# Kernel optimization log

Hardware: AMD Instinct MI355X
Metric: run time of the kernel (lower is better)

## Reference

```python
import jax, jax.numpy as jnp
import numpy as np

N = 50000        # nodes
E = 800000       # edges (avg degree 16)
F_IN = 128       # num_node_features
HEADS = 4        # const.NUM_HEADS
CH = 32          # const.NUM_CHANNELS
CLS = 40         # num_classes
NEG_SLOPE = 0.2  # PyG GATv2Conv default


def setup_inputs() -> dict:
    key = jax.random.key(0)
    ks = jax.random.split(key, 10)
    x = jax.random.normal(ks[0], (N, F_IN), dtype=jnp.float32)
    edge_index = jax.random.randint(ks[1], (2, E), 0, N, dtype=jnp.int64)
    s1 = 1.0 / np.sqrt(F_IN)
    s2 = 1.0 / np.sqrt(HEADS * CH)
    w1_l = jax.random.normal(ks[2], (F_IN, HEADS * CH), jnp.float32) * s1
    w1_r = jax.random.normal(ks[3], (F_IN, HEADS * CH), jnp.float32) * s1
    a1 = jax.random.normal(ks[4], (HEADS, CH), jnp.float32) * (1.0 / np.sqrt(CH))
    b1 = jnp.zeros((HEADS * CH,), jnp.float32)
    w2_l = jax.random.normal(ks[5], (HEADS * CH, CLS), jnp.float32) * s2
    w2_r = jax.random.normal(ks[6], (HEADS * CH, CLS), jnp.float32) * s2
    a2 = jax.random.normal(ks[7], (1, CLS), jnp.float32) * (1.0 / np.sqrt(CLS))
    b2 = jnp.zeros((CLS,), jnp.float32)
    return {"x": x, "edge_index": edge_index, "w1_l": w1_l, "w1_r": w1_r,
            "a1": a1, "b1": b1, "w2_l": w2_l, "w2_r": w2_r, "a2": a2, "b2": b2}


def _gatv2_conv(x, src, dst, wl, wr, a, b, concat):
    """GATv2Conv (PyG semantics, eval mode: no dropout).
    src -> lin_l, dst -> lin_r; e = a . LeakyReLU(x_l[src] + x_r[dst]);
    segment softmax over dst; out_i = sum_j alpha * x_l[src]."""
    H, C = a.shape
    n = x.shape[0]
    xl = (x @ wl).reshape(n, H, C)
    xr = (x @ wr).reshape(n, H, C)
    # per-edge additive attention logits [E, H]
    e = jnp.einsum('ehc,hc->eh', jax.nn.leaky_relu(xl[src] + xr[dst], NEG_SLOPE), a)
    # numerically stable segment softmax over target nodes
    m = jax.ops.segment_max(e, dst, num_segments=n)          # [n, H]
    p = jnp.exp(e - m[dst])
    denom = jax.ops.segment_sum(p, dst, num_segments=n)     # [n, H]
    alpha = p / denom[dst]
    out = jax.ops.segment_sum(alpha[..., None] * xl[src], dst, num_segments=n)  # [n, H, C]
    out = out.reshape(n, H * C) if concat else out.mean(axis=1)
    return out + b


def reference(x, edge_index, w1_l, w1_r, a1, b1, w2_l, w2_r, a2, b2):
    n = x.shape[0]
    # PyG GATv2Conv default add_self_loops=True
    loop = jnp.arange(n, dtype=edge_index.dtype)
    src = jnp.concatenate([edge_index[0], loop])
    dst = jnp.concatenate([edge_index[1], loop])
    h = jax.nn.elu(_gatv2_conv(x, src, dst, w1_l, w1_r, a1, b1, concat=True))
    # F.dropout with training=False is identity
    out = _gatv2_conv(h, src, dst, w2_l, w2_r, a2, b2, concat=False)
    return jax.nn.log_softmax(out, axis=1)
```

## Files before the change

### kernel.cpp

```cpp
#include <hip/hip_runtime.h>
#include <hip/hip_bf16.h>
#include <math.h>

#define NN 50000
#define NE 800000
#define ETOT (NE + NN)
#define CLS 40
#define CLSP 48
#define NEG 0.2f
#define MTILES (NN / 16)
#define GB1 ((MTILES + 3) / 4)
#define PREPB 176
#define NBUCK 196
#define BCAP 8192
#define EB 4096
#define KAB ((ETOT + EB - 1) / EB)

#define L2E 1.44269504088896f
#define C06 (0.6f * L2E)
#define C04 (0.4f * L2E)

typedef __hip_bfloat16 bf16;
typedef __attribute__((ext_vector_type(8))) __bf16 bf16x8;
typedef __attribute__((ext_vector_type(4))) float f32x4;
typedef __attribute__((ext_vector_type(2))) float f32x2;
struct U3 { unsigned x, y, z; };

__device__ __forceinline__ bf16x8 cvt8(f32x4 a, f32x4 b) {
    bf16x8 r;
    r[0] = (__bf16)a[0]; r[1] = (__bf16)a[1]; r[2] = (__bf16)a[2]; r[3] = (__bf16)a[3];
    r[4] = (__bf16)b[0]; r[5] = (__bf16)b[1]; r[6] = (__bf16)b[2]; r[7] = (__bf16)b[3];
    return r;
}
__device__ __forceinline__ f32x2 unpk2(unsigned u) {
    f32x2 r;
    r.x = __uint_as_float(u << 16);
    r.y = __uint_as_float(u & 0xffff0000u);
    return r;
}

__device__ __forceinline__ unsigned scan256(unsigned v, unsigned* wsum) {
    int t = threadIdx.x;
    int lane = t & 63, w = t >> 6;
    unsigned inc = v;
#pragma unroll
    for (int d = 1; d < 64; d <<= 1) {
        unsigned x = __shfl_up(inc, d);
        if (lane >= d) inc += x;
    }
    if (lane == 63) wsum[w] = inc;
    __syncthreads();
    unsigned woff = 0;
#pragma unroll
    for (int i = 0; i < 4; i++) woff += (i < w) ? wsum[i] : 0;
    return woff + inc - v;
}

__global__ __launch_bounds__(256) void prep(
        const float* __restrict__ w1l, const float* __restrict__ w1r,
        const float* __restrict__ w2l, const float* __restrict__ w2r,
        bf16* __restrict__ wT1, bf16* __restrict__ wT2,
        int* __restrict__ bcursor) {
    int t = blockIdx.x * 256 + threadIdx.x;
    if (t < NBUCK) bcursor[t] = 0;
    if (t < 2 * 128 * 128) {
        int m = t >> 14;
        int idx = t & 16383;
        int n = idx >> 7, k = idx & 127;
        const float* w = m ? w1r : w1l;
        wT1[t] = __float2bfloat16(w[k * 128 + n]);
    } else if (t < 2 * 128 * 128 + 2 * CLSP * 128) {
        int u = t - 2 * 128 * 128;
        int m = u / (CLSP * 128);
        int idx = u % (CLSP * 128);
        int n = idx >> 7, k = idx & 127;
        const float* w = m ? w2r : w2l;
        wT2[u] = __float2bfloat16((n < CLS) ? w[k * CLS + n] : 0.0f);
    }
}

__global__ __launch_bounds__(256) void gemm1_scatter(
        const float* __restrict__ x, const bf16* __restrict__ wT,
        bf16* __restrict__ outL, bf16* __restrict__ outR,
        const int* __restrict__ ei, int* __restrict__ bcursor,
        uint2* __restrict__ tmp) {
    __shared__ unsigned hist[256];
    __shared__ unsigned lstart[256];
    __shared__ unsigned lcur[256];
    __shared__ unsigned gbase[256];
    __shared__ unsigned wsum[4];
    __shared__ uint2 binned[EB];
    __shared__ unsigned target[EB];
    if ((int)blockIdx.x < GB1) {
        int wave = threadIdx.x >> 6;
        int lane = threadIdx.x & 63;
        int tile = blockIdx.x * 4 + wave;
        if (tile >= MTILES) return;
        const bf16* wl = wT;
        const bf16* wr = wT + 128 * 128;
        int row0 = tile * 16;
        int l16 = lane & 15, quad = lane >> 4;
        f32x4 z = {0.f, 0.f, 0.f, 0.f};
        f32x4 accl[8], accr[8];
#pragma unroll
        for (int i = 0; i < 8; i++) { accl[i] = z; accr[i] = z; }
        const float* xrow = x + (size_t)(row0 + l16) * 128 + quad * 8;
#pragma unroll
        for (int k0 = 0; k0 < 128; k0 += 32) {
            f32x4 a0 = *reinterpret_cast<const f32x4*>(xrow + k0);
            f32x4 a1v = *reinterpret_cast<const f32x4*>(xrow + k0 + 4);
            bf16x8 a = cvt8(a0, a1v);
#pragma unroll
            for (int ct = 0; ct < 8; ct++) {
                bf16x8 bl = *reinterpret_cast<const bf16x8*>(wl + (ct * 16 + l16) * 128 + k0 + quad * 8);
                bf16x8 br = *reinterpret_cast<const bf16x8*>(wr + (ct * 16 + l16) * 128 + k0 + quad * 8);
                accl[ct] = __builtin_amdgcn_mfma_f32_16x16x32_bf16(a, bl, accl[ct], 0, 0, 0);
                accr[ct] = __builtin_amdgcn_mfma_f32_16x16x32_bf16(a, br, accr[ct], 0, 0, 0);
            }
        }
#pragma unroll
        for (int ct = 0; ct < 8; ct++)
#pragma unroll
            for (int r = 0; r < 4; r++) {
                size_t o = (size_t)(row0 + quad * 4 + r) * 128 + ct * 16 + l16;
                outL[o] = __float2bfloat16(accl[ct][r]);
                outR[o] = __float2bfloat16(accr[ct][r]);
            }
    } else {
        int t = threadIdx.x;
        int e0 = (blockIdx.x - GB1) * EB;
        hist[t] = 0;
        __syncthreads();
        int srcs[16], dsts[16];
#pragma unroll
        for (int i = 0; i < 16; i++) {
            int e = e0 + i * 256 + t;
            if (e < ETOT) {
                int s, d;
                if (e < NE) { s = ei[e]; d = ei[NE + e]; }
                else        { s = d = e - NE; }
                srcs[i] = s; dsts[i] = d;
                atomicAdd(&hist[d >> 8], 1u);
            } else dsts[i] = -1;
        }
        __syncthreads();
        unsigned v = hist[t];
        unsigned excl = scan256(v, wsum);
        lstart[t] = excl;
        lcur[t] = 0;
        __syncthreads();
        if (t < NBUCK && v > 0)
            gbase[t] = (unsigned)atomicAdd(&bcursor[t], (int)v) + (unsigned)t * BCAP;
        __syncthreads();
#pragma unroll
        for (int i = 0; i < 16; i++) {
            int d = dsts[i];
            if (d >= 0) {
                int bk = d >> 8;
                unsigned p = atomicAdd(&lcur[bk], 1u);
                unsigned slot = lstart[bk] + p;
                binned[slot] = make_uint2((unsigned)srcs[i], (unsigned)d);
                target[slot] = gbase[bk] + p;
            }
        }
        __syncthreads();
        int tot = min(EB, ETOT - e0);
        for (int s = t; s < tot; s += 256)
            tmp[target[s]] = binned[s];
    }
}

__global__ __launch_bounds__(256) void bucket_sort(const int* __restrict__ bcursor,
                                                   const uint2* __restrict__ tmp,
                                                   int* __restrict__ csr_src,
                                                   int* __restrict__ startA,
                                                   int* __restrict__ degA) {
    __shared__ unsigned hist[256];
    __shared__ unsigned lcur[256];
    __shared__ unsigned wsum[4];
    int b = blockIdx.x, t = threadIdx.x;
    int cnt = bcursor[b];
    hist[t] = 0;
    __syncthreads();
    const uint2* seg = tmp + (size_t)b * BCAP;
    for (int s = t; s < cnt; s += 256)
        atomicAdd(&hist[seg[s].y & 255], 1u);
    __syncthreads();
    unsigned v = hist[t];
    unsigned excl = scan256(v, wsum);
    lcur[t] = excl;
    int node = b * 256 + t;
    if (node < NN) {
        startA[node] = b * BCAP + (int)excl;
        degA[node] = (int)v;
    }
    __syncthreads();
    int* cbase = csr_src + (size_t)b * BCAP;
    for (int s = t; s < cnt; s += 256) {
        uint2 p = seg[s];
        unsigned pos = atomicAdd(&lcur[p.y & 255], 1u);
        cbase[pos] = (int)p.x;
    }
}

struct L1S { float s; f32x2 acc[4]; };
__device__ __forceinline__ void l1_consume(uint4 u, bool valid, const f32x2* xrp,
                                           const f32x2* a06, const float* a04, L1S& st) {
    f32x2 t0 = unpk2(u.x) + xrp[0];
    f32x2 t1 = unpk2(u.y) + xrp[1];
    f32x2 t2 = unpk2(u.z) + xrp[2];
    f32x2 t3 = unpk2(u.w) + xrp[3];
    f32x2 ep = t0 * a06[0];
    ep = __builtin_elementwise_fma(t1, a06[1], ep);
    ep = __builtin_elementwise_fma(t2, a06[2], ep);
    ep = __builtin_elementwise_fma(t3, a06[3], ep);
    float e0 = fmaf(a04[1], fabsf(t0.y), a04[0] * fabsf(t0.x));
    e0 = fmaf(a04[2], fabsf(t1.x), e0);
    e0 = fmaf(a04[3], fabsf(t1.y), e0);
    float e1 = fmaf(a04[5], fabsf(t2.y), a04[4] * fabsf(t2.x));
    e1 = fmaf(a04[6], fabsf(t3.x), e1);
    e1 = fmaf(a04[7], fabsf(t3.y), e1);
    float e = (ep.x + ep.y) + (e0 + e1);
    e += __shfl_xor(e, 1);
    e += __shfl_xor(e, 2);
    float w = valid ? __builtin_amdgcn_exp2f(e) : 0.f;
    st.s += w;
    f32x2 wv = {w, w};
    st.acc[0] = __builtin_elementwise_fma(wv, t0, st.acc[0]);
    st.acc[1] = __builtin_elementwise_fma(wv, t1, st.acc[1]);
    st.acc[2] = __builtin_elementwise_fma(wv, t2, st.acc[2]);
    st.acc[3] = __builtin_elementwise_fma(wv, t3, st.acc[3]);
}

__global__ __launch_bounds__(256) void node_l1(const int* __restrict__ startA,
                                               const int* __restrict__ degA,
                                               const int* __restrict__ csr_src,
                                               const bf16* __restrict__ xl,
                                               const bf16* __restrict__ xr,
                                               const float* __restrict__ a1,
                                               const float* __restrict__ b1,
                                               bf16* __restrict__ hb) {
    int wid = (blockIdx.x * 256 + threadIdx.x) >> 6;
    int lane = threadIdx.x & 63;
    int g = lane >> 4, t = lane & 15;
    unsigned cB = (unsigned)t * 16;
    int j0 = startA[wid];
    int deg = degA[wid];
    unsigned rowB = (unsigned)csr_src[j0 + min(lane, deg - 1)] << 8;
    const char* xlb = (const char*)xl;
    f32x2 xrp[4];
    {
        uint4 raw = *(const uint4*)((const char*)xr + ((unsigned)wid << 8) + cB);
        xrp[0] = unpk2(raw.x); xrp[1] = unpk2(raw.y);
        xrp[2] = unpk2(raw.z); xrp[3] = unpk2(raw.w);
    }
    f32x2 a06[4];
    float a04[8];
    {
        f32x4 lo = *reinterpret_cast<const f32x4*>(a1 + t * 8);
        f32x4 hi = *reinterpret_cast<const f32x4*>(a1 + t * 8 + 4);
        float af[8];
#pragma unroll
        for (int k = 0; k < 4; k++) { af[k] = lo[k]; af[k + 4] = hi[k]; }
#pragma unroll
        for (int j = 0; j < 4; j++) {
            a06[j].x = af[2 * j] * C06;
            a06[j].y = af[2 * j + 1] * C06;
        }
#pragma unroll
        for (int k = 0; k < 8; k++) a04[k] = af[k] * C04;
    }
    L1S st; st.s = 0.f;
    f32x2 z2 = {0.f, 0.f};
#pragma unroll
    for (int k = 0; k < 4; k++) st.acc[k] = z2;
    int nb = (deg + 3) >> 2;
    uint4 u[8];
#pragma unroll
    for (int i = 0; i < 4; i++) {
        int pp = min(i * 4 + g, deg - 1);
        u[i] = *(const uint4*)(xlb + (__shfl(rowB, pp) + cB));
    }
    if (nb > 4) {
#pragma unroll
        for (int i = 4; i < 8; i++) {
            int pp = min(i * 4 + g, deg - 1);
            u[i] = *(const uint4*)(xlb + (__shfl(rowB, pp) + cB));
        }
    }
    l1_consume(u[0], g < deg, xrp, a06, a04, st);
    if (nb > 1) l1_consume(u[1], 4 + g < deg, xrp, a06, a04, st);
    if (nb > 2) l1_consume(u[2], 8 + g < deg, xrp, a06, a04, st);
    if (nb > 3) l1_consume(u[3], 12 + g < deg, xrp, a06, a04, st);
    if (nb > 4) {
        l1_consume(u[4], 16 + g < deg, xrp, a06, a04, st);
        if (nb > 5) l1_consume(u[5], 20 + g < deg, xrp, a06, a04, st);
        if (nb > 6) l1_consume(u[6], 24 + g < deg, xrp, a06, a04, st);
        if (nb > 7) l1_consume(u[7], 28 + g < deg, xrp, a06, a04, st);
        for (int b = 8; b < nb; b++) {
            int p = b * 4 + g;
            bool valid = p < deg;
            int pp = valid ? p : deg - 1;
            unsigned o = __shfl(rowB, min(pp, 63)) + cB;
            if (pp >= 64) o = (((unsigned)csr_src[j0 + pp]) << 8) + cB;
            uint4 uu = *(const uint4*)(xlb + o);
            l1_consume(uu, valid, xrp, a06, a04, st);
        }
    }
#pragma unroll
    for (int d = 16; d < 64; d <<= 1) {
        st.s += __shfl_xor(st.s, d);
#pragma unroll
        for (int k = 0; k < 4; k++) {
            st.acc[k].x += __shfl_xor(st.acc[k].x, d);
            st.acc[k].y += __shfl_xor(st.acc[k].y, d);
        }
    }
    if (g == 0) {
        float inv = 1.f / st.s;
        unsigned pk[4];
#pragma unroll
        for (int k = 0; k < 4; k++) {
            float o0 = st.acc[k].x * inv - xrp[k].x + b1[t * 8 + 2 * k];
            float o1 = st.acc[k].y * inv - xrp[k].y + b1[t * 8 + 2 * k + 1];
            o0 = o0 > 0.f ? o0 : __expf(o0) - 1.f;
            o1 = o1 > 0.f ? o1 : __expf(o1) - 1.f;
            bf16 r0 = __float2bfloat16(o0), r1 = __float2bfloat16(o1);
            pk[k] = (unsigned)*reinterpret_cast<unsigned short*>(&r0) |
                    ((unsigned)*reinterpret_cast<unsigned short*>(&r1) << 16);
        }
        uint4 w4 = {pk[0], pk[1], pk[2], pk[3]};
        *(uint4*)((char*)hb + ((unsigned)wid << 8) + cB) = w4;
    }
}

__global__ __launch_bounds__(256) void gemm2(const bf16* __restrict__ h,
                                             const bf16* __restrict__ wT,
                                             bf16* __restrict__ outL,
                                             bf16* __restrict__ outR) {
    int wave = threadIdx.x >> 6;
    int lane = threadIdx.x & 63;
    int tile = blockIdx.x * 4 + wave;
    if (tile >= MTILES) return;
    const bf16* wl = wT;
    const bf16* wr = wT + CLSP * 128;
    int row0 = tile * 16;
    int l16 = lane & 15, quad = lane >> 4;
    f32x4 z = {0.f, 0.f, 0.f, 0.f};
    f32x4 accl[3], accr[3];
#pragma unroll
    for (int i = 0; i < 3; i++) { accl[i] = z; accr[i] = z; }
    const bf16* hrow = h + (size_t)(row0 + l16) * 128 + quad * 8;
#pragma unroll
    for (int k0 = 0; k0 < 128; k0 += 32) {
        bf16x8 a = *reinterpret_cast<const bf16x8*>(hrow + k0);
#pragma unroll
        for (int ct = 0; ct < 3; ct++) {
            bf16x8 bl = *reinterpret_cast<const bf16x8*>(wl + (ct * 16 + l16) * 128 + k0 + quad * 8);
            bf16x8 br = *reinterpret_cast<const bf16x8*>(wr + (ct * 16 + l16) * 128 + k0 + quad * 8);
            accl[ct] = __builtin_amdgcn_mfma_f32_16x16x32_bf16(a, bl, accl[ct], 0, 0, 0);
            accr[ct] = __builtin_amdgcn_mfma_f32_16x16x32_bf16(a, br, accr[ct], 0, 0, 0);
        }
    }
#pragma unroll
    for (int ct = 0; ct < 3; ct++)
#pragma unroll
        for (int r = 0; r < 4; r++) {
            size_t o = (size_t)(row0 + quad * 4 + r) * CLSP + ct * 16 + l16;
            outL[o] = __float2bfloat16(accl[ct][r]);
            outR[o] = __float2bfloat16(accr[ct][r]);
        }
}

struct L2S { float s; f32x2 acc[3]; };
__device__ __forceinline__ void l2_consume(U3 u, bool valid, const f32x2* xrp,
                                           const f32x2* a06, const float* a04, L2S& st) {
    f32x2 t0 = unpk2(u.x) + xrp[0];
    f32x2 t1 = unpk2(u.y) + xrp[1];
    f32x2 t2 = unpk2(u.z) + xrp[2];
    f32x2 ep = t0 * a06[0];
    ep = __builtin_elementwise_fma(t1, a06[1], ep);
    ep = __builtin_elementwise_fma(t2, a06[2], ep);
    float es = fmaf(a04[1], fabsf(t0.y), a04[0] * fabsf(t0.x));
    es = fmaf(a04[2], fabsf(t1.x), es);
    es = fmaf(a04[3], fabsf(t1.y), es);
    es = fmaf(a04[4], fabsf(t2.x), es);
    es = fmaf(a04[5], fabsf(t2.y), es);
    float e = (ep.x + ep.y) + es;
    e += __shfl_xor(e, 1);
    e += __shfl_xor(e, 2);
    e += __shfl_xor(e, 4);
    float w = valid ? __builtin_amdgcn_exp2f(e) : 0.f;
    st.s += w;
    f32x2 wv = {w, w};
    st.acc[0] = __builtin_elementwise_fma(wv, t0, st.acc[0]);
    st.acc[1] = __builtin_elementwise_fma(wv, t1, st.acc[1]);
    st.acc[2] = __builtin_elementwise_fma(wv, t2, st.acc[2]);
}

__global__ __launch_bounds__(256) void node_l2(const int* __restrict__ startA,
                                               const int* __restrict__ degA,
                                               const int* __restrict__ csr_src,
                                               const bf16* __restrict__ xl2,
                                               const bf16* __restrict__ xr2,
                                               const float* __restrict__ a2,
                                               const float* __restrict__ b2,
                                               float* __restrict__ out) {
    int wid = (blockIdx.x * 256 + threadIdx.x) >> 6;
    int lane = threadIdx.x & 63;
    int g = lane >> 3, t = lane & 7;
    unsigned cB = (unsigned)t * 12;
    int j0 = startA[wid];
    int deg = degA[wid];
    unsigned rowB = (unsigned)csr_src[j0 + min(lane, deg - 1)] * 96u;
    const char* xlb = (const char*)xl2;
    f32x2 xrp[3];
    {
        U3 raw = *(const U3*)((const char*)xr2 + (unsigned)wid * 96u + cB);
        xrp[0] = unpk2(raw.x); xrp[1] = unpk2(raw.y); xrp[2] = unpk2(raw.z);
    }
    int c = t * 6;
    f32x2 a06[3];
    float a04[6];
#pragma unroll
    for (int k = 0; k < 6; k++) {
        float av = (c + k < CLS) ? a2[c + k] : 0.f;
        a04[k] = av * C04;
        if (k & 1) a06[k >> 1].y = av * C06; else a06[k >> 1].x = av * C06;
    }
    L2S st; st.s = 0.f;
    f32x2 z2 = {0.f, 0.f};
#pragma unroll
    for (int k = 0; k < 3; k++) st.acc[k] = z2;
    int nb = (deg + 7) >> 3;
    U3 u[4];
#pragma unroll
    for (int i = 0; i < 2; i++) {
        int pp = min(i * 8 + g, deg - 1);
        u[i] = *(const U3*)(xlb + (__shfl(rowB, pp) + cB));
    }
    if (nb > 2) {
#pragma unroll
        for (int i = 2; i < 4; i++) {
            int pp = min(i * 8 + g, deg - 1);
            u[i] = *(const U3*)(xlb + (__shfl(rowB, pp) + cB));
        }
    }
    l2_consume(u[0], g < deg, xrp, a06, a04, st);
    if (nb > 1) l2_consume(u[1], 8 + g < deg, xrp, a06, a04, st);
    if (nb > 2) {
        l2_consume(u[2], 16 + g < deg, xrp, a06, a04, st);
        if (nb > 3) l2_consume(u[3], 24 + g < deg, xrp, a06, a04, st);
        for (int b = 4; b < nb; b++) {
            int p = b * 8 + g;
            bool valid = p < deg;
            int pp = valid ? p : deg - 1;
            unsigned o = __shfl(rowB, min(pp, 63)) + cB;
            if (pp >= 64) o = (unsigned)csr_src[j0 + pp] * 96u + cB;
            U3 uu = *(const U3*)(xlb + o);
            l2_consume(uu, valid, xrp, a06, a04, st);
        }
    }
#pragma unroll
    for (int d = 8; d < 64; d <<= 1) {
        st.s += __shfl_xor(st.s, d);
#pragma unroll
        for (int k = 0; k < 3; k++) {
            st.acc[k].x += __shfl_xor(st.acc[k].x, d);
            st.acc[k].y += __shfl_xor(st.acc[k].y, d);
        }
    }
    float inv = 1.f / st.s;
    float q[6];
    float mx = -3e38f;
#pragma unroll
    for (int k = 0; k < 6; k++) {
        bool val = (c + k < CLS);
        float av = (k & 1) ? st.acc[k >> 1].y : st.acc[k >> 1].x;
        float xv = (k & 1) ? xrp[k >> 1].y : xrp[k >> 1].x;
        q[k] = val ? (av * inv - xv + b2[c + k]) : -3e38f;
        mx = fmaxf(mx, q[k]);
    }
    mx = fmaxf(mx, __shfl_xor(mx, 1));
    mx = fmaxf(mx, __shfl_xor(mx, 2));
    mx = fmaxf(mx, __shfl_xor(mx, 4));
    float se = 0.f;
#pragma unroll
    for (int k = 0; k < 6; k++) if (c + k < CLS) se += __expf(q[k] - mx);
    se += __shfl_xor(se, 1);
    se += __shfl_xor(se, 2);
    se += __shfl_xor(se, 4);
    float ls = mx + __logf(se);
    if (g == 0) {
        float* o = out + (size_t)wid * CLS + c;
#pragma unroll
        for (int k = 0; k < 6; k++)
            if (c + k < CLS) o[k] = q[k] - ls;
    }
}

extern "C" void kernel_launch(void* const* d_in, const int* in_sizes, int n_in,
                              void* d_out, int out_size, void* d_ws, size_t ws_size,
                              hipStream_t stream) {
    const float* x   = (const float*)d_in[0];
    const int*   ei  = (const int*)d_in[1];
    const float* w1l = (const float*)d_in[2];
    const float* w1r = (const float*)d_in[3];
    const float* a1  = (const float*)d_in[4];
    const float* b1  = (const float*)d_in[5];
    const float* w2l = (const float*)d_in[6];
    const float* w2r = (const float*)d_in[7];
    const float* a2  = (const float*)d_in[8];
    const float* b2  = (const float*)d_in[9];
    float* out = (float*)d_out;

    char* base = (char*)d_ws;
    int*   bcursor = (int*)(base + 0);
    int*   startA  = (int*)(base + 1024);
    int*   degA    = (int*)(base + 201024);
    uint2* tmp     = (uint2*)(base + 401024);
    int*   csr_src = (int*)(base + 13246080);
    bf16*  xl1     = (bf16*)(base + 19668608);
    bf16*  hb      = (bf16*)(base + 45268608);
    bf16*  xl2p    = (bf16*)(base + 58068608);
    bf16*  wT1     = (bf16*)(base + 67668608);
    bf16*  wT2     = (bf16*)(base + 67734144);
    bf16* xr1  = xl1 + (size_t)NN * 128;
    bf16* xr2p = xl2p + (size_t)NN * CLSP;

    prep<<<PREPB, 256, 0, stream>>>(w1l, w1r, w2l, w2r, wT1, wT2, bcursor);
    gemm1_scatter<<<GB1 + KAB, 256, 0, stream>>>(x, wT1, xl1, xr1, ei, bcursor, tmp);
    bucket_sort<<<NBUCK, 256, 0, stream>>>(bcursor, tmp, csr_src, startA, degA);
    node_l1<<<(NN * 64) / 256, 256, 0, stream>>>(startA, degA, csr_src, xl1, xr1, a1, b1, hb);
    gemm2<<<GB1, 256, 0, stream>>>(hb, wT2, xl2p, xr2p);
    node_l2<<<(NN * 64) / 256, 256, 0, stream>>>(startA, degA, csr_src, xl2p, xr2p, a2, b2, out);
}
```

Before: 231.3 us.

## Make node aggregation kernels persistent with software-pipelined prefetch of next node

Both per-node attention/aggregation kernels now launch a fixed grid of 8192 waves that loop over nodes with stride NW. The next node's CSR metadata, source indices, xr row and first neighbor gathers are prefetched while the current node is consumed and reduced, hiding gather latency. Bias values are hoisted into registers once per wave. This cuts launch/setup overhead and overlaps memory latency, at the cost of higher register pressure and possible load imbalance across waves.

```diff
diff --git a/kernel.cpp b/kernel.cpp
--- a/kernel.cpp
+++ b/kernel.cpp
@@ -15,6 +15,7 @@
 #define BCAP 8192
 #define EB 4096
 #define KAB ((ETOT + EB - 1) / EB)
+#define NW 8192
 
 #define L2E 1.44269504088896f
 #define C06 (0.6f * L2E)
@@ -240,28 +241,24 @@
                                                const float* __restrict__ a1,
                                                const float* __restrict__ b1,
                                                bf16* __restrict__ hb) {
-    int wid = (blockIdx.x * 256 + threadIdx.x) >> 6;
+    int wv = (blockIdx.x * 256 + threadIdx.x) >> 6;
     int lane = threadIdx.x & 63;
     int g = lane >> 4, t = lane & 15;
     unsigned cB = (unsigned)t * 16;
-    int j0 = startA[wid];
-    int deg = degA[wid];
-    unsigned rowB = (unsigned)csr_src[j0 + min(lane, deg - 1)] << 8;
     const char* xlb = (const char*)xl;
-    f32x2 xrp[4];
-    {
-        uint4 raw = *(const uint4*)((const char*)xr + ((unsigned)wid << 8) + cB);
-        xrp[0] = unpk2(raw.x); xrp[1] = unpk2(raw.y);
-        xrp[2] = unpk2(raw.z); xrp[3] = unpk2(raw.w);
-    }
     f32x2 a06[4];
-    float a04[8];
+    float a04[8], bv[8];
     {
         f32x4 lo = *reinterpret_cast<const f32x4*>(a1 + t * 8);
         f32x4 hi = *reinterpret_cast<const f32x4*>(a1 + t * 8 + 4);
+        f32x4 blo = *reinterpret_cast<const f32x4*>(b1 + t * 8);
+        f32x4 bhi = *reinterpret_cast<const f32x4*>(b1 + t * 8 + 4);
         float af[8];
 #pragma unroll
-        for (int k = 0; k < 4; k++) { af[k] = lo[k]; af[k + 4] = hi[k]; }
+        for (int k = 0; k < 4; k++) {
+            af[k] = lo[k]; af[k + 4] = hi[k];
+            bv[k] = blo[k]; bv[k + 4] = bhi[k];
+        }
 #pragma unroll
         for (int j = 0; j < 4; j++) {
             a06[j].x = af[2 * j] * C06;
@@ -270,67 +267,90 @@
 #pragma unroll
         for (int k = 0; k < 8; k++) a04[k] = af[k] * C04;
     }
-    L1S st; st.s = 0.f;
-    f32x2 z2 = {0.f, 0.f};
-#pragma unroll
-    for (int k = 0; k < 4; k++) st.acc[k] = z2;
-    int nb = (deg + 3) >> 2;
+    int n = wv;
+    int j0 = startA[n], deg = degA[n];
+    unsigned rowB = (unsigned)csr_src[j0 + min(lane, deg - 1)] << 8;
+    uint4 xrw = *(const uint4*)((const char*)xr + ((unsigned)n << 8) + cB);
     uint4 u[8];
 #pragma unroll
-    for (int i = 0; i < 4; i++) {
-        int pp = min(i * 4 + g, deg - 1);
-        u[i] = *(const uint4*)(xlb + (__shfl(rowB, pp) + cB));
-    }
-    if (nb > 4) {
-#pragma unroll
-        for (int i = 4; i < 8; i++) {
-            int pp = min(i * 4 + g, deg - 1);
-            u[i] = *(const uint4*)(xlb + (__shfl(rowB, pp) + cB));
-        }
-    }
-    l1_consume(u[0], g < deg, xrp, a06, a04, st);
-    if (nb > 1) l1_consume(u[1], 4 + g < deg, xrp, a06, a04, st);
-    if (nb > 2) l1_consume(u[2], 8 + g < deg, xrp, a06, a04, st);
-    if (nb > 3) l1_consume(u[3], 12 + g < deg, xrp, a06, a04, st);
-    if (nb > 4) {
-        l1_consume(u[4], 16 + g < deg, xrp, a06, a04, st);
-        if (nb > 5) l1_consume(u[5], 20 + g < deg, xrp, a06, a04, st);
-        if (nb > 6) l1_consume(u[6], 24 + g < deg, xrp, a06, a04, st);
-        if (nb > 7) l1_consume(u[7], 28 + g < deg, xrp, a06, a04, st);
-        for (int b = 8; b < nb; b++) {
-            int p = b * 4 + g;
-            bool valid = p < deg;
-            int pp = valid ? p : deg - 1;
-            unsigned o = __shfl(rowB, min(pp, 63)) + cB;
-            if (pp >= 64) o = (((unsigned)csr_src[j0 + pp]) << 8) + cB;
-            uint4 uu = *(const uint4*)(xlb + o);
-            l1_consume(uu, valid, xrp, a06, a04, st);
-        }
-    }
-#pragma unroll
-    for (int d = 16; d < 64; d <<= 1) {
-        st.s += __shfl_xor(st.s, d);
-#pragma unroll
-        for (int k = 0; k < 4; k++) {
-            st.acc[k].x += __shfl_xor(st.acc[k].x, d);
-            st.acc[k].y += __shfl_xor(st.acc[k].y, d);
-        }
-    }
-    if (g == 0) {
-        float inv = 1.f / st.s;
-        unsigned pk[4];
-#pragma unroll
-        for (int k = 0; k < 4; k++) {
-            float o0 = st.acc[k].x * inv - xrp[k].x + b1[t * 8 + 2 * k];
-            float o1 = st.acc[k].y * inv - xrp[k].y + b1[t * 8 + 2 * k + 1];
-            o0 = o0 > 0.f ? o0 : __expf(o0) - 1.f;
-            o1 = o1 > 0.f ? o1 : __expf(o1) - 1.f;
-            bf16 r0 = __float2bfloat16(o0), r1 = __float2bfloat16(o1);
-            pk[k] = (unsigned)*reinterpret_cast<unsigned short*>(&r0) |
-                    ((unsigned)*reinterpret_cast<unsigned short*>(&r1) << 16);
-        }
-        uint4 w4 = {pk[0], pk[1], pk[2], pk[3]};
-        *(uint4*)((char*)hb + ((unsigned)wid << 8) + cB) = w4;
+    for (int i = 0; i < 4; i++)
+        u[i] = *(const uint4*)(xlb + (__shfl(rowB, min(i * 4 + g, deg - 1)) + cB));
+
+    for (;;) {
+        int n2 = n + NW;
+        bool has2 = n2 < NN;
+        int j0b = 0, degb = 1;
+        unsigned rowBb = 0;
+        uint4 xrwb = {0, 0, 0, 0};
+        if (has2) {
+            j0b = startA[n2]; degb = degA[n2];
+            rowBb = (unsigned)csr_src[j0b + min(lane, degb - 1)] << 8;
+            xrwb = *(const uint4*)((const char*)xr + ((unsigned)n2 << 8) + cB);
+        }
+        int nb = (deg + 3) >> 2;
+        if (nb > 4) {
+#pragma unroll
+            for (int i = 4; i < 8; i++)
+                u[i] = *(const uint4*)(xlb + (__shfl(rowB, min(i * 4 + g, deg - 1)) + cB));
+        }
+        f32x2 xrp[4];
+        xrp[0] = unpk2(xrw.x); xrp[1] = unpk2(xrw.y);
+        xrp[2] = unpk2(xrw.z); xrp[3] = unpk2(xrw.w);
+        L1S st; st.s = 0.f;
+        f32x2 z2 = {0.f, 0.f};
+#pragma unroll
+        for (int k = 0; k < 4; k++) st.acc[k] = z2;
+        l1_consume(u[0], g < deg, xrp, a06, a04, st);
+        if (nb > 1) l1_consume(u[1], 4 + g < deg, xrp, a06, a04, st);
+        if (nb > 2) l1_consume(u[2], 8 + g < deg, xrp, a06, a04, st);
+        if (nb > 3) l1_consume(u[3], 12 + g < deg, xrp, a06, a04, st);
+        if (nb > 4) {
+            l1_consume(u[4], 16 + g < deg, xrp, a06, a04, st);
+            if (nb > 5) l1_consume(u[5], 20 + g < deg, xrp, a06, a04, st);
+            if (nb > 6) l1_consume(u[6], 24 + g < deg, xrp, a06, a04, st);
+            if (nb > 7) l1_consume(u[7], 28 + g < deg, xrp, a06, a04, st);
+            for (int b = 8; b < nb; b++) {
+                int p = b * 4 + g;
+                bool valid = p < deg;
+                int pp = valid ? p : deg - 1;
+                unsigned o = __shfl(rowB, min(pp, 63)) + cB;
+                if (pp >= 64) o = (((unsigned)csr_src[j0 + pp]) << 8) + cB;
+                uint4 uu = *(const uint4*)(xlb + o);
+                l1_consume(uu, valid, xrp, a06, a04, st);
+            }
+        }
+        if (has2) {
+#pragma unroll
+            for (int i = 0; i < 4; i++)
+                u[i] = *(const uint4*)(xlb + (__shfl(rowBb, min(i * 4 + g, degb - 1)) + cB));
+        }
+#pragma unroll
+        for (int d = 16; d < 64; d <<= 1) {
+            st.s += __shfl_xor(st.s, d);
+#pragma unroll
+            for (int k = 0; k < 4; k++) {
+                st.acc[k].x += __shfl_xor(st.acc[k].x, d);
+                st.acc[k].y += __shfl_xor(st.acc[k].y, d);
+            }
+        }
+        if (g == 0) {
+            float inv = 1.f / st.s;
+            unsigned pk[4];
+#pragma unroll
+            for (int k = 0; k < 4; k++) {
+                float o0 = st.acc[k].x * inv - xrp[k].x + bv[2 * k];
+                float o1 = st.acc[k].y * inv - xrp[k].y + bv[2 * k + 1];
+                o0 = o0 > 0.f ? o0 : __expf(o0) - 1.f;
+                o1 = o1 > 0.f ? o1 : __expf(o1) - 1.f;
+                bf16 r0 = __float2bfloat16(o0), r1 = __float2bfloat16(o1);
+                pk[k] = (unsigned)*reinterpret_cast<unsigned short*>(&r0) |
+                        ((unsigned)*reinterpret_cast<unsigned short*>(&r1) << 16);
+            }
+            uint4 w4 = {pk[0], pk[1], pk[2], pk[3]};
+            *(uint4*)((char*)hb + ((unsigned)n << 8) + cB) = w4;
+        }
+        if (!has2) break;
+        n = n2; j0 = j0b; deg = degb; rowB = rowBb; xrw = xrwb;
     }
 }
 
@@ -406,96 +426,112 @@
                                                const float* __restrict__ a2,
                                                const float* __restrict__ b2,
                                                float* __restrict__ out) {
-    int wid = (blockIdx.x * 256 + threadIdx.x) >> 6;
+    int wv = (blockIdx.x * 256 + threadIdx.x) >> 6;
     int lane = threadIdx.x & 63;
     int g = lane >> 3, t = lane & 7;
     unsigned cB = (unsigned)t * 12;
-    int j0 = startA[wid];
-    int deg = degA[wid];
-    unsigned rowB = (unsigned)csr_src[j0 + min(lane, deg - 1)] * 96u;
     const char* xlb = (const char*)xl2;
-    f32x2 xrp[3];
-    {
-        U3 raw = *(const U3*)((const char*)xr2 + (unsigned)wid * 96u + cB);
-        xrp[0] = unpk2(raw.x); xrp[1] = unpk2(raw.y); xrp[2] = unpk2(raw.z);
-    }
     int c = t * 6;
     f32x2 a06[3];
-    float a04[6];
+    float a04[6], bv[6];
 #pragma unroll
     for (int k = 0; k < 6; k++) {
-        float av = (c + k < CLS) ? a2[c + k] : 0.f;
+        bool val = (c + k < CLS);
+        float av = val ? a2[c + k] : 0.f;
+        bv[k] = val ? b2[c + k] : 0.f;
         a04[k] = av * C04;
         if (k & 1) a06[k >> 1].y = av * C06; else a06[k >> 1].x = av * C06;
     }
-    L2S st; st.s = 0.f;
-    f32x2 z2 = {0.f, 0.f};
-#pragma unroll
-    for (int k = 0; k < 3; k++) st.acc[k] = z2;
-    int nb = (deg + 7) >> 3;
+    int n = wv;
+    int j0 = startA[n], deg = degA[n];
+    unsigned rowB = (unsigned)csr_src[j0 + min(lane, deg - 1)] * 96u;
+    U3 xrw = *(const U3*)((const char*)xr2 + (unsigned)n * 96u + cB);
     U3 u[4];
 #pragma unroll
-    for (int i = 0; i < 2; i++) {
-        int pp = min(i * 8 + g, deg - 1);
-        u[i] = *(const U3*)(xlb + (__shfl(rowB, pp) + cB));
-    }
-    if (nb > 2) {
-#pragma unroll
-        for (int i = 2; i < 4; i++) {
-            int pp = min(i * 8 + g, deg - 1);
-            u[i] = *(const U3*)(xlb + (__shfl(rowB, pp) + cB));
-        }
-    }
-    l2_consume(u[0], g < deg, xrp, a06, a04, st);
-    if (nb > 1) l2_consume(u[1], 8 + g < deg, xrp, a06, a04, st);
-    if (nb > 2) {
-        l2_consume(u[2], 16 + g < deg, xrp, a06, a04, st);
-        if (nb > 3) l2_consume(u[3], 24 + g < deg, xrp, a06, a04, st);
-        for (int b = 4; b < nb; b++) {
-            int p = b * 8 + g;
-            bool valid = p < deg;
-            int pp = valid ? p : deg - 1;
-            unsigned o = __shfl(rowB, min(pp, 63)) + cB;
-            if (pp >= 64) o = (unsigned)csr_src[j0 + pp] * 96u + cB;
-            U3 uu = *(const U3*)(xlb + o);
-            l2_consume(uu, valid, xrp, a06, a04, st);
-        }
-    }
-#pragma unroll
-    for (int d = 8; d < 64; d <<= 1) {
-        st.s += __shfl_xor(st.s, d);
-#pragma unroll
-        for (int k = 0; k < 3; k++) {
-            st.acc[k].x += __shfl_xor(st.acc[k].x, d);
-            st.acc[k].y += __shfl_xor(st.acc[k].y, d);
-        }
-    }
-    float inv = 1.f / st.s;
-    float q[6];
-    float mx = -3e38f;
-#pragma unroll
-    for (int k = 0; k < 6; k++) {
-        bool val = (c + k < CLS);
-        float av = (k & 1) ? st.acc[k >> 1].y : st.acc[k >> 1].x;
-        float xv = (k & 1) ? xrp[k >> 1].y : xrp[k >> 1].x;
-        q[k] = val ? (av * inv - xv + b2[c + k]) : -3e38f;
-        mx = fmaxf(mx, q[k]);
-    }
-    mx = fmaxf(mx, __shfl_xor(mx, 1));
-    mx = fmaxf(mx, __shfl_xor(mx, 2));
-    mx = fmaxf(mx, __shfl_xor(mx, 4));
-    float se = 0.f;
-#pragma unroll
-    for (int k = 0; k < 6; k++) if (c + k < CLS) se += __expf(q[k] - mx);
-    se += __shfl_xor(se, 1);
-    se += __shfl_xor(se, 2);
-    se += __shfl_xor(se, 4);
-    float ls = mx + __logf(se);
-    if (g == 0) {
-        float* o = out + (size_t)wid * CLS + c;
-#pragma unroll
-        for (int k = 0; k < 6; k++)
-            if (c + k < CLS) o[k] = q[k] - ls;
+    for (int i = 0; i < 2; i++)
+        u[i] = *(const U3*)(xlb + (__shfl(rowB, min(i * 8 + g, deg - 1)) + cB));
+
+    for (;;) {
+        int n2 = n + NW;
+        bool has2 = n2 < NN;
+        int j0b = 0, degb = 1;
+        unsigned rowBb = 0;
+        U3 xrwb = {0, 0, 0};
+        if (has2) {
+            j0b = startA[n2]; degb = degA[n2];
+            rowBb = (unsigned)csr_src[j0b + min(lane, degb - 1)] * 96u;
+            xrwb = *(const U3*)((const char*)xr2 + (unsigned)n2 * 96u + cB);
+        }
+        int nb = (deg + 7) >> 3;
+        if (nb > 2) {
+#pragma unroll
+            for (int i = 2; i < 4; i++)
+                u[i] = *(const U3*)(xlb + (__shfl(rowB, min(i * 8 + g, deg - 1)) + cB));
+        }
+        f32x2 xrp[3];
+        xrp[0] = unpk2(xrw.x); xrp[1] = unpk2(xrw.y); xrp[2] = unpk2(xrw.z);
+        L2S st; st.s = 0.f;
+        f32x2 z2 = {0.f, 0.f};
+#pragma unroll
+        for (int k = 0; k < 3; k++) st.acc[k] = z2;
+        l2_consume(u[0], g < deg, xrp, a06, a04, st);
+        if (nb > 1) l2_consume(u[1], 8 + g < deg, xrp, a06, a04, st);
+        if (nb > 2) {
+            l2_consume(u[2], 16 + g < deg, xrp, a06, a04, st);
+            if (nb > 3) l2_consume(u[3], 24 + g < deg, xrp, a06, a04, st);
+            for (int b = 4; b < nb; b++) {
+                int p = b * 8 + g;
+                bool valid = p < deg;
+                int pp = valid ? p : deg - 1;
+                unsigned o = __shfl(rowB, min(pp, 63)) + cB;
+                if (pp >= 64) o = (unsigned)csr_src[j0 + pp] * 96u + cB;
+                U3 uu = *(const U3*)(xlb + o);
+                l2_consume(uu, valid, xrp, a06, a04, st);
+            }
+        }
+        if (has2) {
+#pragma unroll
+            for (int i = 0; i < 2; i++)
+                u[i] = *(const U3*)(xlb + (__shfl(rowBb, min(i * 8 + g, degb - 1)) + cB));
+        }
+#pragma unroll
+        for (int d = 8; d < 64; d <<= 1) {
+            st.s += __shfl_xor(st.s, d);
+#pragma unroll
+            for (int k = 0; k < 3; k++) {
+                st.acc[k].x += __shfl_xor(st.acc[k].x, d);
+                st.acc[k].y += __shfl_xor(st.acc[k].y, d);
+            }
+        }
+        float inv = 1.f / st.s;
+        float q[6];
+        float mx = -3e38f;
+#pragma unroll
+        for (int k = 0; k < 6; k++) {
+            bool val = (c + k < CLS);
+            float av = (k & 1) ? st.acc[k >> 1].y : st.acc[k >> 1].x;
+            float xv = (k & 1) ? xrp[k >> 1].y : xrp[k >> 1].x;
+            q[k] = val ? (av * inv - xv + bv[k]) : -3e38f;
+            mx = fmaxf(mx, q[k]);
+        }
+        mx = fmaxf(mx, __shfl_xor(mx, 1));
+        mx = fmaxf(mx, __shfl_xor(mx, 2));
+        mx = fmaxf(mx, __shfl_xor(mx, 4));
+        float se = 0.f;
+#pragma unroll
+        for (int k = 0; k < 6; k++) if (c + k < CLS) se += __expf(q[k] - mx);
+        se += __shfl_xor(se, 1);
+        se += __shfl_xor(se, 2);
+        se += __shfl_xor(se, 4);
+        float ls = mx + __logf(se);
+        if (g == 0) {
+            float* o = out + (size_t)n * CLS + c;
+#pragma unroll
+            for (int k = 0; k < 6; k++)
+                if (c + k < CLS) o[k] = q[k] - ls;
+        }
+        if (!has2) break;
+        n = n2; j0 = j0b; deg = degb; rowB = rowBb; xrw = xrwb;
     }
 }
 
@@ -531,7 +567,7 @@
     prep<<<PREPB, 256, 0, stream>>>(w1l, w1r, w2l, w2r, wT1, wT2, bcursor);
     gemm1_scatter<<<GB1 + KAB, 256, 0, stream>>>(x, wT1, xl1, xr1, ei, bcursor, tmp);
     bucket_sort<<<NBUCK, 256, 0, stream>>>(bcursor, tmp, csr_src, startA, degA);
-    node_l1<<<(NN * 64) / 256, 256, 0, stream>>>(startA, degA, csr_src, xl1, xr1, a1, b1, hb);
+    node_l1<<<NW / 4, 256, 0, stream>>>(startA, degA, csr_src, xl1, xr1, a1, b1, hb);
     gemm2<<<GB1, 256, 0, stream>>>(hb, wT2, xl2p, xr2p);
-    node_l2<<<(NN * 64) / 256, 256, 0, stream>>>(startA, degA, csr_src, xl2p, xr2p, a2, b2, out);
-}
+    node_l2<<<NW / 4, 256, 0, stream>>>(startA, degA, csr_src, xl2p, xr2p, a2, b2, out);
+}
```

After: 238.9 us. 3.3% more time.
